# Kernel optimization log

Hardware: AMD Instinct MI355X
Metric: run time of the kernel (lower is better)

Reference implementation:

```python
import jax, jax.numpy as jnp
import numpy as np

C = 256
RED = 2
C2 = C // RED


def setup_inputs() -> dict:
    key = jax.random.key(0)
    ks = jax.random.split(key, 6)
    B, H, W = 8, 64, 64
    x = jax.random.normal(ks[0], (B, C, H, W), dtype=jnp.float32)
    # 1x1 convs stored as [out_ch, in_ch] matrices
    W1 = jax.random.normal(ks[1], (C2, C), dtype=jnp.float32) * (1.0 / np.sqrt(C))
    b1 = jax.random.normal(ks[2], (C2,), dtype=jnp.float32) * 0.01
    W2 = jax.random.normal(ks[3], (C, C2), dtype=jnp.float32) * (1.0 / np.sqrt(C2))
    b2 = jax.random.normal(ks[4], (C,), dtype=jnp.float32) * 0.01
    # torch inits scale to zeros; use randn so the residual branch is active
    scale = jax.random.normal(ks[5], (1, C, 1, 1), dtype=jnp.float32)
    return {"x": x, "W1": W1, "b1": b1, "W2": W2, "b2": b2, "scale": scale}


def reference(x, W1, b1, W2, b2, scale):
    B, Cc, H, Wd = x.shape
    # conv1 (1x1): [B,C,H,W] -> [B,C2,H,W]
    y = jnp.einsum('bchw,oc->bohw', x, W1) + b1[None, :, None, None]
    # flatten spatial, move channels last: [B, N, C2]
    y = y.reshape(B, C2, H * Wd).transpose(0, 2, 1)
    # unscaled self-attention over N spatial positions
    att = jax.nn.softmax(jnp.einsum('bmc,bnc->bmn', y, y), axis=-1)  # [B,N,N]
    out = jnp.einsum('bmn,bnc->bmc', att, y)  # [B,N,C2]
    # faithful to torch: raw .view(B,-1,H,W) WITHOUT permuting back
    out = out.reshape(B, C2, H, Wd)
    # conv2 (1x1): [B,C2,H,W] -> [B,C,H,W]
    out = jnp.einsum('bchw,oc->bohw', out, W2) + b2[None, :, None, None]
    return out * scale + x
```

## Files before the change

kernel.cpp:

```cpp
#include <hip/hip_runtime.h>

#define B_  8
#define C_  256
#define C2_ 128
#define N_  4096
#define LOG2E 1.44269504088896f

typedef _Float16 f16;
typedef _Float16 f16x8 __attribute__((ext_vector_type(8)));
typedef float f32x4  __attribute__((ext_vector_type(4)));

__global__ __launch_bounds__(256)
void prep_kernel(const float* __restrict__ W1, const float* __restrict__ W2,
                 f16* __restrict__ w1h, f16* __restrict__ w2h)
{
  int i = blockIdx.x * 256 + threadIdx.x;
  w1h[i] = (f16)W1[i];
  w2h[i] = (f16)W2[i];
}

__global__ __launch_bounds__(256, 3)
void conv1_kernel(const float* __restrict__ x,
                  const f16* __restrict__ w1h,
                  const float* __restrict__ b1,
                  f16* __restrict__ Y, f16* __restrict__ Yt)
{
  __shared__ __align__(16) char smem[49152];
  float* Xr = (float*)smem;
  f16*   Ah = (f16*)(smem + 32768);
  f16*   T  = (f16*)smem;

  const int t = threadIdx.x;
  const int w = t >> 6, lane = t & 63, quad = lane >> 4, l16 = lane & 15;
  const int b = blockIdx.x, nt0 = blockIdx.y;

#pragma unroll
  for (int pass = 0; pass < 8; pass++) {
    int c  = (t >> 3) + pass * 32;
    int n4 = t & 7;
    float4 v = *(const float4*)(x + ((long)(b * C_ + c)) * N_ + nt0 * 32 + n4 * 4);
    *(float4*)(&Xr[c * 32 + (n4 ^ (c & 7)) * 4]) = v;
  }
  __syncthreads();
#pragma unroll
  for (int pass = 0; pass < 4; pass++) {
    int n  = t & 31;
    int kb = (t >> 5) + pass * 8;
    f16x8 vh;
#pragma unroll
    for (int jj = 0; jj < 8; jj++) {
      int cc = kb * 8 + jj;
      vh[jj] = (f16)Xr[cc * 32 + ((n >> 2) ^ (cc & 7)) * 4 + (n & 3)];
    }
    *(f16x8*)(&Ah[n * 256 + (kb ^ (n & 7)) * 8]) = vh;
  }
  __syncthreads();

  f16x8 bh[2][8];
#pragma unroll
  for (int nt = 0; nt < 2; nt++) {
    int c2 = w * 32 + nt * 16 + l16;
#pragma unroll
    for (int ks = 0; ks < 8; ks++)
      bh[nt][ks] = *(const f16x8*)(w1h + c2 * C_ + ks * 32 + quad * 8);
  }

  f32x4 acc[2][2];
#pragma unroll
  for (int i = 0; i < 2; i++)
#pragma unroll
    for (int j = 0; j < 2; j++) acc[i][j] = (f32x4){0.f, 0.f, 0.f, 0.f};

#pragma unroll
  for (int ks = 0; ks < 8; ks++)
#pragma unroll
    for (int mt = 0; mt < 2; mt++) {
      f16x8 ah = *(const f16x8*)(&Ah[(mt * 16 + l16) * 256 + (((ks * 4 + quad) ^ (l16 & 7))) * 8]);
#pragma unroll
      for (int nt = 0; nt < 2; nt++)
        acc[mt][nt] = __builtin_amdgcn_mfma_f32_16x16x32_f16(ah, bh[nt][ks], acc[mt][nt], 0, 0, 0);
    }
  __syncthreads();

#pragma unroll
  for (int nt = 0; nt < 2; nt++) {
    int c2 = w * 32 + nt * 16 + l16;
    float bv = b1[c2];
#pragma unroll
    for (int mt = 0; mt < 2; mt++)
#pragma unroll
      for (int rg = 0; rg < 4; rg++) {
        int n = mt * 16 + quad * 4 + rg;
        T[c2 * 40 + n] = (f16)(acc[mt][nt][rg] + bv);
      }
  }
  __syncthreads();
#pragma unroll
  for (int pass = 0; pass < 2; pass++) {
    int r  = (t >> 2) + pass * 64;
    int c8 = (t & 3) * 8;
    f16x8 v = *(const f16x8*)(&T[r * 40 + c8]);
    *(f16x8*)(Yt + ((long)(b * C2_ + r)) * N_ + nt0 * 32 + c8) = v;
  }
#pragma unroll
  for (int pass = 0; pass < 2; pass++) {
    int row = t & 31;
    int cg  = (t >> 5) + pass * 8;
    f16x8 v;
#pragma unroll
    for (int jj = 0; jj < 8; jj++) v[jj] = T[(cg * 8 + jj) * 40 + row];
    *(f16x8*)(Y + ((long)(b * N_ + nt0 * 32 + row)) * C2_ + cg * 8) = v;
  }
}

__global__ __launch_bounds__(256, 2)
void attn_kernel(const f16* __restrict__ Y, const f16* __restrict__ Yt,
                 f16* __restrict__ Op, float* __restrict__ ls)
{
  __shared__ f16 Ks[64 * 128];
  __shared__ f16 Vs[128 * 64];
  __shared__ f16 Ps[128 * 64];

  const int t = threadIdx.x;
  const int w = t >> 6, lane = t & 63, quad = lane >> 4, l16 = lane & 15;
  const int b = blockIdx.x, qt = blockIdx.y, s = blockIdx.z;
  const f16* Yb  = Y  + (long)b * N_ * C2_;
  const f16* Ytb = Yt + (long)b * C2_ * N_;
  const int kbase0 = s * 2048;

  f16x8 qf[2][4];
#pragma unroll
  for (int mt = 0; mt < 2; mt++)
#pragma unroll
    for (int ks = 0; ks < 4; ks++)
      qf[mt][ks] = *(const f16x8*)(Yb + (long)(qt * 128 + w * 32 + mt * 16 + l16) * C2_ + ks * 32 + quad * 8);

  {
    float* nsqf = (float*)Ps;
    int r = t >> 1, half = t & 1;
    float ss = 0.f;
#pragma unroll
    for (int j = 0; j < 8; j++) {
      f16x8 v = *(const f16x8*)(Yb + (long)(qt * 128 + r) * C2_ + half * 64 + j * 8);
#pragma unroll
      for (int e = 0; e < 8; e++) { float f = (float)v[e]; ss = fmaf(f, f, ss); }
    }
    ss += __shfl_xor(ss, 1);
    if (!(t & 1)) nsqf[r] = ss;
  }

#pragma unroll
  for (int pass = 0; pass < 4; pass++) {
    int r = (t >> 4) + pass * 16;
    f16x8 kv = *(const f16x8*)(Yb + (long)(kbase0 + r) * C2_ + (t & 15) * 8);
    *(f16x8*)(&Ks[r * 128 + (((t & 15)) ^ (r & 15)) * 8]) = kv;
  }
#pragma unroll
  for (int pass = 0; pass < 4; pass++) {
    int d = (t >> 3) + pass * 32;
    f16x8 vv = *(const f16x8*)(Ytb + (long)d * N_ + kbase0 + (t & 7) * 8);
    *(f16x8*)(&Vs[d * 64 + (((t & 7)) ^ (d & 7)) * 8]) = vv;
  }
  __syncthreads();

  float myns[2][4];
  {
    const float* nsqf = (const float*)Ps;
#pragma unroll
    for (int mt = 0; mt < 2; mt++)
#pragma unroll
      for (int rg = 0; rg < 4; rg++)
        myns[mt][rg] = nsqf[w * 32 + mt * 16 + quad * 4 + rg] * LOG2E;
  }
  __syncthreads();

  f16x8 ones;
#pragma unroll
  for (int j = 0; j < 8; j++) ones[j] = (f16)1.0f;

  f32x4 Oa[2][8];
#pragma unroll
  for (int i = 0; i < 2; i++)
#pragma unroll
    for (int j = 0; j < 8; j++) Oa[i][j] = (f32x4){0.f, 0.f, 0.f, 0.f};
  f32x4 lac[2] = {(f32x4){0.f,0.f,0.f,0.f}, (f32x4){0.f,0.f,0.f,0.f}};

#pragma unroll 1
  for (int kt = 0; kt < 32; kt++) {
    f16x8 stK[4], stV[4];
    if (kt + 1 < 32) {
      int nb = kbase0 + (kt + 1) * 64;
#pragma unroll
      for (int pass = 0; pass < 4; pass++)
        stK[pass] = *(const f16x8*)(Yb + (long)(nb + (t >> 4) + pass * 16) * C2_ + (t & 15) * 8);
#pragma unroll
      for (int pass = 0; pass < 4; pass++)
        stV[pass] = *(const f16x8*)(Ytb + (long)((t >> 3) + pass * 32) * N_ + nb + (t & 7) * 8);
    }

    f32x4 S[2][4];
#pragma unroll
    for (int i = 0; i < 2; i++)
#pragma unroll
      for (int j = 0; j < 4; j++) S[i][j] = (f32x4){0.f, 0.f, 0.f, 0.f};
#pragma unroll
    for (int ks = 0; ks < 4; ks++) {
      f16x8 bfr[4];
#pragma unroll
      for (int nt = 0; nt < 4; nt++)
        bfr[nt] = *(const f16x8*)(&Ks[(nt * 16 + l16) * 128 + (((ks * 4 + quad) ^ l16)) * 8]);
#pragma unroll
      for (int mt = 0; mt < 2; mt++)
#pragma unroll
        for (int nt = 0; nt < 4; nt++)
          S[mt][nt] = __builtin_amdgcn_mfma_f32_16x16x32_f16(qf[mt][ks], bfr[nt], S[mt][nt], 0, 0, 0);
    }

#pragma unroll
    for (int mt = 0; mt < 2; mt++)
#pragma unroll
      for (int rg = 0; rg < 4; rg++) {
        float nm = myns[mt][rg];
        int r = w * 32 + mt * 16 + quad * 4 + rg;
#pragma unroll
        for (int nt = 0; nt < 4; nt++) {
          float p = exp2f(fminf(fmaf(S[mt][nt][rg], LOG2E, -nm), 11.0f));
          int col = nt * 16 + l16;
          Ps[r * 64 + (((col >> 3) ^ (r & 7))) * 8 + (col & 7)] = (f16)p;
        }
      }

#pragma unroll
    for (int ks2 = 0; ks2 < 2; ks2++) {
      f16x8 vb[8];
#pragma unroll
      for (int dt = 0; dt < 8; dt++)
        vb[dt] = *(const f16x8*)(&Vs[(dt * 16 + l16) * 64 + (((ks2 * 4 + quad) ^ (l16 & 7))) * 8]);
      f16x8 pa[2];
#pragma unroll
      for (int mt = 0; mt < 2; mt++)
        pa[mt] = *(const f16x8*)(&Ps[(w * 32 + mt * 16 + l16) * 64 + (((ks2 * 4 + quad) ^ (l16 & 7))) * 8]);
#pragma unroll
      for (int mt = 0; mt < 2; mt++) {
#pragma unroll
        for (int dt = 0; dt < 8; dt++)
          Oa[mt][dt] = __builtin_amdgcn_mfma_f32_16x16x32_f16(pa[mt], vb[dt], Oa[mt][dt], 0, 0, 0);
        lac[mt] = __builtin_amdgcn_mfma_f32_16x16x32_f16(pa[mt], ones, lac[mt], 0, 0, 0);
      }
    }

    __syncthreads();
    if (kt + 1 < 32) {
#pragma unroll
      for (int pass = 0; pass < 4; pass++) {
        int r = (t >> 4) + pass * 16;
        *(f16x8*)(&Ks[r * 128 + (((t & 15)) ^ (r & 15)) * 8]) = stK[pass];
      }
#pragma unroll
      for (int pass = 0; pass < 4; pass++) {
        int d = (t >> 3) + pass * 32;
        *(f16x8*)(&Vs[d * 64 + (((t & 7)) ^ (d & 7)) * 8]) = stV[pass];
      }
    }
    __syncthreads();
  }

  const long rbase = ((long)s * B_ + b) * N_ + qt * 128;
#pragma unroll
  for (int mt = 0; mt < 2; mt++)
#pragma unroll
    for (int rg = 0; rg < 4; rg++) {
      int r = w * 32 + mt * 16 + quad * 4 + rg;
#pragma unroll
      for (int dt = 0; dt < 8; dt++)
        Op[(rbase + r) * C2_ + dt * 16 + l16] = (f16)Oa[mt][dt][rg];
      if (l16 == 0) ls[rbase + r] = lac[mt][rg];
    }
}

__global__ __launch_bounds__(256, 4)
void conv2_kernel(const f16* __restrict__ Op, const float* __restrict__ ls,
                  const f16* __restrict__ w2h,
                  const float* __restrict__ b2,
                  const float* __restrict__ scale,
                  const float* __restrict__ x,
                  float* __restrict__ out)
{
  __shared__ f16 Or[128 * 72];
  __shared__ f16 Bsw[64 * 128];
  __shared__ float invL[128];

  const int t = threadIdx.x;
  const int w = t >> 6, lane = t & 63, quad = lane >> 4, l16 = lane & 15;
  const int b = blockIdx.x, pt = blockIdx.y, oh = blockIdx.z;
  const long base0 = (long)b * 524288;
  const long base1 = 4194304 + base0;

  if (t < 128) {
    int q = t * 32 + (pt >> 1);
    float l = ls[(long)b * N_ + q] + ls[32768 + (long)b * N_ + q];
    invL[t] = 1.0f / fmaxf(l, 1e-20f);
  }
  __syncthreads();

#pragma unroll
  for (int pass = 0; pass < 4; pass++) {
    int j = (t >> 3) + pass * 32;
    int c8 = (t & 7) * 8;
    f16x8 a0 = *(const f16x8*)(Op + base0 + (long)j * N_ + pt * 64 + c8);
    f16x8 a1 = *(const f16x8*)(Op + base1 + (long)j * N_ + pt * 64 + c8);
    float iv = invL[j];
    f16x8 r;
#pragma unroll
    for (int jj = 0; jj < 8; jj++)
      r[jj] = (f16)(((float)a0[jj] + (float)a1[jj]) * iv);
    *(f16x8*)(&Or[j * 72 + c8]) = r;
  }
  __syncthreads();
#pragma unroll
  for (int pass = 0; pass < 4; pass++) {
    int p = t & 63;
    int q = (t >> 6) + pass * 4;
    f16x8 vv;
#pragma unroll
    for (int jj = 0; jj < 8; jj++) vv[jj] = Or[(q * 8 + jj) * 72 + p];
    *(f16x8*)(&Bsw[p * 128 + ((q ^ (p & 15))) * 8]) = vv;
  }
  __syncthreads();

  f32x4 acc[2][4];
#pragma unroll
  for (int i = 0; i < 2; i++)
#pragma unroll
    for (int j = 0; j < 4; j++) acc[i][j] = (f32x4){0.f, 0.f, 0.f, 0.f};

#pragma unroll
  for (int ks = 0; ks < 4; ks++) {
    f16x8 bfr[4];
#pragma unroll
    for (int nt = 0; nt < 4; nt++)
      bfr[nt] = *(const f16x8*)(&Bsw[(nt * 16 + l16) * 128 + (((ks * 4 + quad) ^ l16)) * 8]);
#pragma unroll
    for (int mt = 0; mt < 2; mt++) {
      int o = oh * 128 + w * 32 + mt * 16 + l16;
      f16x8 ah = *(const f16x8*)(w2h + o * C2_ + ks * 32 + quad * 8);
#pragma unroll
      for (int nt = 0; nt < 4; nt++)
        acc[mt][nt] = __builtin_amdgcn_mfma_f32_16x16x32_f16(ah, bfr[nt], acc[mt][nt], 0, 0, 0);
    }
  }
#pragma unroll
  for (int mt = 0; mt < 2; mt++)
#pragma unroll
    for (int rg = 0; rg < 4; rg++) {
      int o = oh * 128 + w * 32 + mt * 16 + quad * 4 + rg;
      float so = scale[o], bo = b2[o];
#pragma unroll
      for (int nt = 0; nt < 4; nt++) {
        int p = pt * 64 + nt * 16 + l16;
        long xo = ((long)b * C_ + o) * N_ + p;
        out[xo] = (acc[mt][nt][rg] + bo) * so + x[xo];
      }
    }
}

extern "C" void kernel_launch(void* const* d_in, const int* in_sizes, int n_in,
                              void* d_out, int out_size, void* d_ws, size_t ws_size,
                              hipStream_t stream) {
  const float* x     = (const float*)d_in[0];
  const float* W1    = (const float*)d_in[1];
  const float* b1    = (const float*)d_in[2];
  const float* W2    = (const float*)d_in[3];
  const float* b2    = (const float*)d_in[4];
  const float* scale = (const float*)d_in[5];
  float* outp = (float*)d_out;

  const size_t NE = (size_t)B_ * N_ * C2_;
  f16* Y   = (f16*)d_ws;
  f16* Yt  = Y + NE;
  f16* Op  = Yt + NE;
  float* ls = (float*)(Op + 2 * NE);
  f16* w1h = (f16*)(ls + 65536);
  f16* w2h = w1h + 32768;

  prep_kernel <<<dim3(128),      dim3(256), 0, stream>>>(W1, W2, w1h, w2h);
  conv1_kernel<<<dim3(8, 128),   dim3(256), 0, stream>>>(x, w1h, b1, Y, Yt);
  attn_kernel <<<dim3(8, 32, 2), dim3(256), 0, stream>>>(Y, Yt, Op, ls);
  conv2_kernel<<<dim3(8, 64, 2), dim3(256), 0, stream>>>(Op, ls, w2h, b2, scale, x, outp);
}
```

Before: 220.1 us.

## Raise attention key-split count based on workspace and shrink conv1 shared memory

The attention kernel now splits the key range across a runtime-chosen number of blocks (up to 4, depending on workspace size) instead of a fixed 2. This raises the grid from 512 blocks toward 1024, aiming to fill more CUs, and occupancy hints are raised. conv2 sums a variable number of partial outputs and normalisers, which adds more global reads and merge traffic. conv1 stages x in two channel halves to halve its shared memory and loads W1 fragments per k-step, allowing 4 blocks per CU.

```diff
diff --git a/kernel.cpp b/kernel.cpp
--- a/kernel.cpp
+++ b/kernel.cpp
@@ -19,50 +19,44 @@
   w2h[i] = (f16)W2[i];
 }
 
-__global__ __launch_bounds__(256, 3)
+__global__ __launch_bounds__(256, 4)
 void conv1_kernel(const float* __restrict__ x,
                   const f16* __restrict__ w1h,
                   const float* __restrict__ b1,
                   f16* __restrict__ Y, f16* __restrict__ Yt)
 {
-  __shared__ __align__(16) char smem[49152];
+  __shared__ __align__(16) char smem[32768];
   float* Xr = (float*)smem;
-  f16*   Ah = (f16*)(smem + 32768);
+  f16*   Ah = (f16*)(smem + 16384);
   f16*   T  = (f16*)smem;
 
   const int t = threadIdx.x;
   const int w = t >> 6, lane = t & 63, quad = lane >> 4, l16 = lane & 15;
   const int b = blockIdx.x, nt0 = blockIdx.y;
 
-#pragma unroll
-  for (int pass = 0; pass < 8; pass++) {
-    int c  = (t >> 3) + pass * 32;
-    int n4 = t & 7;
-    float4 v = *(const float4*)(x + ((long)(b * C_ + c)) * N_ + nt0 * 32 + n4 * 4);
-    *(float4*)(&Xr[c * 32 + (n4 ^ (c & 7)) * 4]) = v;
-  }
-  __syncthreads();
-#pragma unroll
-  for (int pass = 0; pass < 4; pass++) {
-    int n  = t & 31;
-    int kb = (t >> 5) + pass * 8;
-    f16x8 vh;
-#pragma unroll
-    for (int jj = 0; jj < 8; jj++) {
-      int cc = kb * 8 + jj;
-      vh[jj] = (f16)Xr[cc * 32 + ((n >> 2) ^ (cc & 7)) * 4 + (n & 3)];
-    }
-    *(f16x8*)(&Ah[n * 256 + (kb ^ (n & 7)) * 8]) = vh;
-  }
-  __syncthreads();
-
-  f16x8 bh[2][8];
-#pragma unroll
-  for (int nt = 0; nt < 2; nt++) {
-    int c2 = w * 32 + nt * 16 + l16;
-#pragma unroll
-    for (int ks = 0; ks < 8; ks++)
-      bh[nt][ks] = *(const f16x8*)(w1h + c2 * C_ + ks * 32 + quad * 8);
+#pragma unroll 1
+  for (int kc = 0; kc < 2; kc++) {
+#pragma unroll
+    for (int pass = 0; pass < 4; pass++) {
+      int c  = (t >> 3) + pass * 32;
+      int n4 = t & 7;
+      float4 v = *(const float4*)(x + ((long)(b * C_ + kc * 128 + c)) * N_ + nt0 * 32 + n4 * 4);
+      *(float4*)(&Xr[c * 32 + (n4 ^ (c & 7)) * 4]) = v;
+    }
+    __syncthreads();
+#pragma unroll
+    for (int pass = 0; pass < 2; pass++) {
+      int n   = t & 31;
+      int kbl = (t >> 5) + pass * 8;
+      f16x8 vh;
+#pragma unroll
+      for (int jj = 0; jj < 8; jj++) {
+        int cc = kbl * 8 + jj;
+        vh[jj] = (f16)Xr[cc * 32 + ((n >> 2) ^ (cc & 7)) * 4 + (n & 3)];
+      }
+      *(f16x8*)(&Ah[n * 256 + ((kc * 16 + kbl) ^ (n & 7)) * 8]) = vh;
+    }
+    __syncthreads();
   }
 
   f32x4 acc[2][2];
@@ -72,15 +66,21 @@
     for (int j = 0; j < 2; j++) acc[i][j] = (f32x4){0.f, 0.f, 0.f, 0.f};
 
 #pragma unroll
-  for (int ks = 0; ks < 8; ks++)
+  for (int ks = 0; ks < 8; ks++) {
+    f16x8 bh[2];
+#pragma unroll
+    for (int nt = 0; nt < 2; nt++) {
+      int c2 = w * 32 + nt * 16 + l16;
+      bh[nt] = *(const f16x8*)(w1h + c2 * C_ + ks * 32 + quad * 8);
+    }
 #pragma unroll
     for (int mt = 0; mt < 2; mt++) {
       f16x8 ah = *(const f16x8*)(&Ah[(mt * 16 + l16) * 256 + (((ks * 4 + quad) ^ (l16 & 7))) * 8]);
 #pragma unroll
       for (int nt = 0; nt < 2; nt++)
-        acc[mt][nt] = __builtin_amdgcn_mfma_f32_16x16x32_f16(ah, bh[nt][ks], acc[mt][nt], 0, 0, 0);
-    }
-  __syncthreads();
+        acc[mt][nt] = __builtin_amdgcn_mfma_f32_16x16x32_f16(ah, bh[nt], acc[mt][nt], 0, 0, 0);
+    }
+  }
 
 #pragma unroll
   for (int nt = 0; nt < 2; nt++) {
@@ -113,7 +113,7 @@
   }
 }
 
-__global__ __launch_bounds__(256, 2)
+__global__ __launch_bounds__(256, 3)
 void attn_kernel(const f16* __restrict__ Y, const f16* __restrict__ Yt,
                  f16* __restrict__ Op, float* __restrict__ ls)
 {
@@ -124,9 +124,14 @@
   const int t = threadIdx.x;
   const int w = t >> 6, lane = t & 63, quad = lane >> 4, l16 = lane & 15;
   const int b = blockIdx.x, qt = blockIdx.y, s = blockIdx.z;
+  const int ns = gridDim.z;
+  const int per = 64 / ns, rem = 64 % ns;
+  const int cnt = per + (s < rem ? 1 : 0);
+  const int st  = s * per + (s < rem ? s : rem);
+  const int kbase0 = st * 64;
+
   const f16* Yb  = Y  + (long)b * N_ * C2_;
   const f16* Ytb = Yt + (long)b * C2_ * N_;
-  const int kbase0 = s * 2048;
 
   f16x8 qf[2][4];
 #pragma unroll
@@ -186,9 +191,9 @@
   f32x4 lac[2] = {(f32x4){0.f,0.f,0.f,0.f}, (f32x4){0.f,0.f,0.f,0.f}};
 
 #pragma unroll 1
-  for (int kt = 0; kt < 32; kt++) {
+  for (int kt = 0; kt < cnt; kt++) {
     f16x8 stK[4], stV[4];
-    if (kt + 1 < 32) {
+    if (kt + 1 < cnt) {
       int nb = kbase0 + (kt + 1) * 64;
 #pragma unroll
       for (int pass = 0; pass < 4; pass++)
@@ -250,7 +255,7 @@
     }
 
     __syncthreads();
-    if (kt + 1 < 32) {
+    if (kt + 1 < cnt) {
 #pragma unroll
       for (int pass = 0; pass < 4; pass++) {
         int r = (t >> 4) + pass * 16;
@@ -284,7 +289,7 @@
                   const float* __restrict__ b2,
                   const float* __restrict__ scale,
                   const float* __restrict__ x,
-                  float* __restrict__ out)
+                  float* __restrict__ out, int ns)
 {
   __shared__ f16 Or[128 * 72];
   __shared__ f16 Bsw[64 * 128];
@@ -293,12 +298,12 @@
   const int t = threadIdx.x;
   const int w = t >> 6, lane = t & 63, quad = lane >> 4, l16 = lane & 15;
   const int b = blockIdx.x, pt = blockIdx.y, oh = blockIdx.z;
-  const long base0 = (long)b * 524288;
-  const long base1 = 4194304 + base0;
 
   if (t < 128) {
     int q = t * 32 + (pt >> 1);
-    float l = ls[(long)b * N_ + q] + ls[32768 + (long)b * N_ + q];
+    float l = 0.f;
+#pragma unroll 1
+    for (int ss = 0; ss < ns; ss++) l += ls[(long)ss * 32768 + (long)b * N_ + q];
     invL[t] = 1.0f / fmaxf(l, 1e-20f);
   }
   __syncthreads();
@@ -307,13 +312,17 @@
   for (int pass = 0; pass < 4; pass++) {
     int j = (t >> 3) + pass * 32;
     int c8 = (t & 7) * 8;
-    f16x8 a0 = *(const f16x8*)(Op + base0 + (long)j * N_ + pt * 64 + c8);
-    f16x8 a1 = *(const f16x8*)(Op + base1 + (long)j * N_ + pt * 64 + c8);
+    float s8[8] = {0.f,0.f,0.f,0.f,0.f,0.f,0.f,0.f};
+#pragma unroll 1
+    for (int ss = 0; ss < ns; ss++) {
+      f16x8 a = *(const f16x8*)(Op + ((long)ss * B_ + b) * ((long)N_ * C2_) + (long)j * N_ + pt * 64 + c8);
+#pragma unroll
+      for (int jj = 0; jj < 8; jj++) s8[jj] += (float)a[jj];
+    }
     float iv = invL[j];
     f16x8 r;
 #pragma unroll
-    for (int jj = 0; jj < 8; jj++)
-      r[jj] = (f16)(((float)a0[jj] + (float)a1[jj]) * iv);
+    for (int jj = 0; jj < 8; jj++) r[jj] = (f16)(s8[jj] * iv);
     *(f16x8*)(&Or[j * 72 + c8]) = r;
   }
   __syncthreads();
@@ -376,15 +385,20 @@
   float* outp = (float*)d_out;
 
   const size_t NE = (size_t)B_ * N_ * C2_;
-  f16* Y   = (f16*)d_ws;
-  f16* Yt  = Y + NE;
-  f16* Op  = Yt + NE;
-  float* ls = (float*)(Op + 2 * NE);
-  f16* w1h = (f16*)(ls + 65536);
-  f16* w2h = w1h + 32768;
-
-  prep_kernel <<<dim3(128),      dim3(256), 0, stream>>>(W1, W2, w1h, w2h);
-  conv1_kernel<<<dim3(8, 128),   dim3(256), 0, stream>>>(x, w1h, b1, Y, Yt);
-  attn_kernel <<<dim3(8, 32, 2), dim3(256), 0, stream>>>(Y, Yt, Op, ls);
-  conv2_kernel<<<dim3(8, 64, 2), dim3(256), 0, stream>>>(Op, ls, w2h, b2, scale, x, outp);
+  f16* Y    = (f16*)d_ws;
+  f16* Yt   = Y + NE;
+  f16* w1h  = Yt + NE;
+  f16* w2h  = w1h + 32768;
+  float* ls = (float*)(w2h + 32768);
+  f16* Op   = (f16*)(ls + 4 * 32768);
+
+  size_t fixed = (size_t)((char*)Op - (char*)d_ws);
+  int ns = 2;
+  if (ws_size >= fixed + 4 * NE * sizeof(f16)) ns = 4;
+  else if (ws_size >= fixed + 3 * NE * sizeof(f16)) ns = 3;
+
+  prep_kernel <<<dim3(128),       dim3(256), 0, stream>>>(W1, W2, w1h, w2h);
+  conv1_kernel<<<dim3(8, 128),    dim3(256), 0, stream>>>(x, w1h, b1, Y, Yt);
+  attn_kernel <<<dim3(8, 32, ns), dim3(256), 0, stream>>>(Y, Yt, Op, ls);
+  conv2_kernel<<<dim3(8, 64, 2),  dim3(256), 0, stream>>>(Op, ls, w2h, b2, scale, x, outp, ns);
 }
```

After: 585.7 us. 166% more time.

## Double-buffer attention K/V tiles and pack P stores via permuted V layout

Applied to the files above, without the earlier changes.

The attention loop now ping-pongs between two K/V shared-memory buffers, so the barrier before writing the next tile is dropped. The softmax probabilities are stored to LDS as packed 4-element vectors instead of scalars. To keep P·V correct, conv1 writes the transposed Y in a key-permuted order within each 64-key block that matches the new P column order. Conv1 also stages x in two halves to halve its shared memory and raise its occupancy hint. The costs are doubled K/V LDS in the attention kernel and scalar strided stores for the permuted transpose in conv1.

```diff
diff --git a/kernel.cpp b/kernel.cpp
--- a/kernel.cpp
+++ b/kernel.cpp
@@ -8,7 +8,9 @@
 
 typedef _Float16 f16;
 typedef _Float16 f16x8 __attribute__((ext_vector_type(8)));
+typedef _Float16 f16x4 __attribute__((ext_vector_type(4)));
 typedef float f32x4  __attribute__((ext_vector_type(4)));
+
 
 __global__ __launch_bounds__(256)
 void prep_kernel(const float* __restrict__ W1, const float* __restrict__ W2,
@@ -19,50 +21,50 @@
   w2h[i] = (f16)W2[i];
 }
 
-__global__ __launch_bounds__(256, 3)
+__global__ __launch_bounds__(256, 4)
 void conv1_kernel(const float* __restrict__ x,
                   const f16* __restrict__ w1h,
                   const float* __restrict__ b1,
-                  f16* __restrict__ Y, f16* __restrict__ Yt)
+                  f16* __restrict__ Y, f16* __restrict__ Ytp)
 {
-  __shared__ __align__(16) char smem[49152];
+  __shared__ __align__(16) char smem[32768];
   float* Xr = (float*)smem;
-  f16*   Ah = (f16*)(smem + 32768);
+  f16*   Ah = (f16*)(smem + 16384);
   f16*   T  = (f16*)smem;
 
   const int t = threadIdx.x;
   const int w = t >> 6, lane = t & 63, quad = lane >> 4, l16 = lane & 15;
   const int b = blockIdx.x, nt0 = blockIdx.y;
 
-#pragma unroll
-  for (int pass = 0; pass < 8; pass++) {
-    int c  = (t >> 3) + pass * 32;
-    int n4 = t & 7;
-    float4 v = *(const float4*)(x + ((long)(b * C_ + c)) * N_ + nt0 * 32 + n4 * 4);
-    *(float4*)(&Xr[c * 32 + (n4 ^ (c & 7)) * 4]) = v;
-  }
-  __syncthreads();
-#pragma unroll
-  for (int pass = 0; pass < 4; pass++) {
-    int n  = t & 31;
-    int kb = (t >> 5) + pass * 8;
-    f16x8 vh;
-#pragma unroll
-    for (int jj = 0; jj < 8; jj++) {
-      int cc = kb * 8 + jj;
-      vh[jj] = (f16)Xr[cc * 32 + ((n >> 2) ^ (cc & 7)) * 4 + (n & 3)];
-    }
-    *(f16x8*)(&Ah[n * 256 + (kb ^ (n & 7)) * 8]) = vh;
-  }
-  __syncthreads();
-
-  f16x8 bh[2][8];
-#pragma unroll
-  for (int nt = 0; nt < 2; nt++) {
-    int c2 = w * 32 + nt * 16 + l16;
-#pragma unroll
-    for (int ks = 0; ks < 8; ks++)
-      bh[nt][ks] = *(const f16x8*)(w1h + c2 * C_ + ks * 32 + quad * 8);
+  const int cr = t >> 3, n4 = (t & 7) * 4;
+  float4 va[4], vb4[4];
+#pragma unroll
+  for (int pass = 0; pass < 4; pass++)
+    va[pass] = *(const float4*)(x + ((long)(b * C_ + cr + pass * 32)) * N_ + nt0 * 32 + n4);
+#pragma unroll
+  for (int pass = 0; pass < 4; pass++)
+    vb4[pass] = *(const float4*)(x + ((long)(b * C_ + 128 + cr + pass * 32)) * N_ + nt0 * 32 + n4);
+
+#pragma unroll 1
+  for (int kc = 0; kc < 2; kc++) {
+#pragma unroll
+    for (int pass = 0; pass < 4; pass++) {
+      int c = cr + pass * 32;
+      *(float4*)(&Xr[c * 32 + ((t & 7) ^ (c & 7)) * 4]) = kc ? vb4[pass] : va[pass];
+    }
+    __syncthreads();
+#pragma unroll
+    for (int pass = 0; pass < 2; pass++) {
+      int n = t & 31, kbl = (t >> 5) + pass * 8;
+      f16x8 vh;
+#pragma unroll
+      for (int jj = 0; jj < 8; jj++) {
+        int cc = kbl * 8 + jj;
+        vh[jj] = (f16)Xr[cc * 32 + ((n >> 2) ^ (cc & 7)) * 4 + (n & 3)];
+      }
+      *(f16x8*)(&Ah[n * 256 + ((kc * 16 + kbl) ^ (n & 7)) * 8]) = vh;
+    }
+    __syncthreads();
   }
 
   f32x4 acc[2][2];
@@ -72,15 +74,21 @@
     for (int j = 0; j < 2; j++) acc[i][j] = (f32x4){0.f, 0.f, 0.f, 0.f};
 
 #pragma unroll
-  for (int ks = 0; ks < 8; ks++)
+  for (int ks = 0; ks < 8; ks++) {
+    f16x8 bh[2];
+#pragma unroll
+    for (int nt = 0; nt < 2; nt++) {
+      int c2 = w * 32 + nt * 16 + l16;
+      bh[nt] = *(const f16x8*)(w1h + c2 * C_ + ks * 32 + quad * 8);
+    }
 #pragma unroll
     for (int mt = 0; mt < 2; mt++) {
       f16x8 ah = *(const f16x8*)(&Ah[(mt * 16 + l16) * 256 + (((ks * 4 + quad) ^ (l16 & 7))) * 8]);
 #pragma unroll
       for (int nt = 0; nt < 2; nt++)
-        acc[mt][nt] = __builtin_amdgcn_mfma_f32_16x16x32_f16(ah, bh[nt][ks], acc[mt][nt], 0, 0, 0);
-    }
-  __syncthreads();
+        acc[mt][nt] = __builtin_amdgcn_mfma_f32_16x16x32_f16(ah, bh[nt], acc[mt][nt], 0, 0, 0);
+    }
+  }
 
 #pragma unroll
   for (int nt = 0; nt < 2; nt++) {
@@ -97,10 +105,13 @@
   __syncthreads();
 #pragma unroll
   for (int pass = 0; pass < 2; pass++) {
-    int r  = (t >> 2) + pass * 64;
-    int c8 = (t & 3) * 8;
-    f16x8 v = *(const f16x8*)(&T[r * 40 + c8]);
-    *(f16x8*)(Yt + ((long)(b * C2_ + r)) * N_ + nt0 * 32 + c8) = v;
+    int r   = (t >> 2) + pass * 64;
+    int nlb = (t & 3) * 8;
+    f16* dst = Ytp + ((long)(b * C2_ + r)) * N_ + (nt0 >> 1) * 64
+             + (nt0 & 1) * 2 + (nlb >> 4);
+#pragma unroll
+    for (int j = 0; j < 8; j++)
+      dst[((nlb & 15) + j) * 4] = T[r * 40 + nlb + j];
   }
 #pragma unroll
   for (int pass = 0; pass < 2; pass++) {
@@ -114,19 +125,20 @@
 }
 
 __global__ __launch_bounds__(256, 2)
-void attn_kernel(const f16* __restrict__ Y, const f16* __restrict__ Yt,
+void attn_kernel(const f16* __restrict__ Y, const f16* __restrict__ Ytp,
                  f16* __restrict__ Op, float* __restrict__ ls)
 {
-  __shared__ f16 Ks[64 * 128];
-  __shared__ f16 Vs[128 * 64];
+  __shared__ f16 Ks[2 * 64 * 128];
+  __shared__ f16 Vs[2 * 128 * 64];
   __shared__ f16 Ps[128 * 64];
 
   const int t = threadIdx.x;
   const int w = t >> 6, lane = t & 63, quad = lane >> 4, l16 = lane & 15;
   const int b = blockIdx.x, qt = blockIdx.y, s = blockIdx.z;
-  const f16* Yb  = Y  + (long)b * N_ * C2_;
-  const f16* Ytb = Yt + (long)b * C2_ * N_;
   const int kbase0 = s * 2048;
+
+  const f16* Yb   = Y   + (long)b * N_ * C2_;
+  const f16* Ytpb = Ytp + (long)b * C2_ * N_;
 
   f16x8 qf[2][4];
 #pragma unroll
@@ -158,7 +170,7 @@
 #pragma unroll
   for (int pass = 0; pass < 4; pass++) {
     int d = (t >> 3) + pass * 32;
-    f16x8 vv = *(const f16x8*)(Ytb + (long)d * N_ + kbase0 + (t & 7) * 8);
+    f16x8 vv = *(const f16x8*)(Ytpb + (long)d * N_ + kbase0 + (t & 7) * 8);
     *(f16x8*)(&Vs[d * 64 + (((t & 7)) ^ (d & 7)) * 8]) = vv;
   }
   __syncthreads();
@@ -187,6 +199,11 @@
 
 #pragma unroll 1
   for (int kt = 0; kt < 32; kt++) {
+    f16* Kc = &Ks[(kt & 1) * 8192];
+    f16* Vc = &Vs[(kt & 1) * 8192];
+    f16* Kn = &Ks[((kt + 1) & 1) * 8192];
+    f16* Vn = &Vs[((kt + 1) & 1) * 8192];
+
     f16x8 stK[4], stV[4];
     if (kt + 1 < 32) {
       int nb = kbase0 + (kt + 1) * 64;
@@ -195,7 +212,7 @@
         stK[pass] = *(const f16x8*)(Yb + (long)(nb + (t >> 4) + pass * 16) * C2_ + (t & 15) * 8);
 #pragma unroll
       for (int pass = 0; pass < 4; pass++)
-        stV[pass] = *(const f16x8*)(Ytb + (long)((t >> 3) + pass * 32) * N_ + nb + (t & 7) * 8);
+        stV[pass] = *(const f16x8*)(Ytpb + (long)((t >> 3) + pass * 32) * N_ + nb + (t & 7) * 8);
     }
 
     f32x4 S[2][4];
@@ -208,7 +225,7 @@
       f16x8 bfr[4];
 #pragma unroll
       for (int nt = 0; nt < 4; nt++)
-        bfr[nt] = *(const f16x8*)(&Ks[(nt * 16 + l16) * 128 + (((ks * 4 + quad) ^ l16)) * 8]);
+        bfr[nt] = *(const f16x8*)(&Kc[(nt * 16 + l16) * 128 + (((ks * 4 + quad) ^ l16)) * 8]);
 #pragma unroll
       for (int mt = 0; mt < 2; mt++)
 #pragma unroll
@@ -222,12 +239,11 @@
       for (int rg = 0; rg < 4; rg++) {
         float nm = myns[mt][rg];
         int r = w * 32 + mt * 16 + quad * 4 + rg;
-#pragma unroll
-        for (int nt = 0; nt < 4; nt++) {
-          float p = exp2f(fminf(fmaf(S[mt][nt][rg], LOG2E, -nm), 11.0f));
-          int col = nt * 16 + l16;
-          Ps[r * 64 + (((col >> 3) ^ (r & 7))) * 8 + (col & 7)] = (f16)p;
-        }
+        f16x4 pk;
+#pragma unroll
+        for (int nt = 0; nt < 4; nt++)
+          pk[nt] = (f16)exp2f(fminf(fmaf(S[mt][nt][rg], LOG2E, -nm), 11.0f));
+        *(f16x4*)(&Ps[r * 64 + ((l16 >> 1) ^ (r & 7)) * 8 + (l16 & 1) * 4]) = pk;
       }
 
 #pragma unroll
@@ -235,7 +251,7 @@
       f16x8 vb[8];
 #pragma unroll
       for (int dt = 0; dt < 8; dt++)
-        vb[dt] = *(const f16x8*)(&Vs[(dt * 16 + l16) * 64 + (((ks2 * 4 + quad) ^ (l16 & 7))) * 8]);
+        vb[dt] = *(const f16x8*)(&Vc[(dt * 16 + l16) * 64 + (((ks2 * 4 + quad) ^ (l16 & 7))) * 8]);
       f16x8 pa[2];
 #pragma unroll
       for (int mt = 0; mt < 2; mt++)
@@ -249,17 +265,16 @@
       }
     }
 
-    __syncthreads();
     if (kt + 1 < 32) {
 #pragma unroll
       for (int pass = 0; pass < 4; pass++) {
         int r = (t >> 4) + pass * 16;
-        *(f16x8*)(&Ks[r * 128 + (((t & 15)) ^ (r & 15)) * 8]) = stK[pass];
+        *(f16x8*)(&Kn[r * 128 + (((t & 15)) ^ (r & 15)) * 8]) = stK[pass];
       }
 #pragma unroll
       for (int pass = 0; pass < 4; pass++) {
         int d = (t >> 3) + pass * 32;
-        *(f16x8*)(&Vs[d * 64 + (((t & 7)) ^ (d & 7)) * 8]) = stV[pass];
+        *(f16x8*)(&Vn[d * 64 + (((t & 7)) ^ (d & 7)) * 8]) = stV[pass];
       }
     }
     __syncthreads();
@@ -293,8 +308,8 @@
   const int t = threadIdx.x;
   const int w = t >> 6, lane = t & 63, quad = lane >> 4, l16 = lane & 15;
   const int b = blockIdx.x, pt = blockIdx.y, oh = blockIdx.z;
-  const long base0 = (long)b * 524288;
-  const long base1 = 4194304 + base0;
+  const long base0 = (long)b * ((long)N_ * C2_);
+  const long base1 = (long)B_ * N_ * C2_ + base0;
 
   if (t < 128) {
     int q = t * 32 + (pt >> 1);
@@ -376,15 +391,15 @@
   float* outp = (float*)d_out;
 
   const size_t NE = (size_t)B_ * N_ * C2_;
-  f16* Y   = (f16*)d_ws;
-  f16* Yt  = Y + NE;
-  f16* Op  = Yt + NE;
-  float* ls = (float*)(Op + 2 * NE);
-  f16* w1h = (f16*)(ls + 65536);
-  f16* w2h = w1h + 32768;
+  f16* Y    = (f16*)d_ws;
+  f16* Ytp  = Y + NE;
+  f16* w1h  = Ytp + NE;
+  f16* w2h  = w1h + 32768;
+  float* ls = (float*)(w2h + 32768);
+  f16* Op   = (f16*)(ls + 2 * 32768);
 
   prep_kernel <<<dim3(128),      dim3(256), 0, stream>>>(W1, W2, w1h, w2h);
-  conv1_kernel<<<dim3(8, 128),   dim3(256), 0, stream>>>(x, w1h, b1, Y, Yt);
-  attn_kernel <<<dim3(8, 32, 2), dim3(256), 0, stream>>>(Y, Yt, Op, ls);
+  conv1_kernel<<<dim3(8, 128),   dim3(256), 0, stream>>>(x, w1h, b1, Y, Ytp);
+  attn_kernel <<<dim3(8, 32, 2), dim3(256), 0, stream>>>(Y, Ytp, Op, ls);
   conv2_kernel<<<dim3(8, 64, 2), dim3(256), 0, stream>>>(Op, ls, w2h, b2, scale, x, outp);
 }
```

Result: slower. 232.5 us (+5.6%).
